# Optimization experiments

Hardware: AMD Instinct MI355X
Metric: run time of the kernel (lower is better)

The kernel has to match this reference:

```python
import jax, jax.numpy as jnp
import numpy as np

WIN = 7
K1, K2 = 0.01, 0.03


def _box_filter(x, w):
    """Valid-padding uniform box filter. x: (B, D, H, W); w: (1, 1, k, k)."""
    B, D, H, Wd = x.shape
    k = w.shape[-1]
    y = jax.lax.conv_general_dilated(
        x.reshape(B * D, 1, H, Wd), w, window_strides=(1, 1), padding='VALID',
        dimension_numbers=('NCHW', 'OIHW', 'NCHW'))
    return y.reshape(B, D, H - k + 1, Wd - k + 1)


def setup_inputs() -> dict:
    key = jax.random.key(0)
    kx, ky = jax.random.split(key)
    X = jax.random.uniform(kx, (4, 64, 256, 256), dtype=jnp.float32)
    Y = jax.random.uniform(ky, (4, 64, 256, 256), dtype=jnp.float32)
    w = jnp.ones((1, 1, WIN, WIN), dtype=jnp.float32) / (WIN * WIN)  # buffer self.w
    return {"X": X, "Y": Y, "w": w}


def reference(X, Y, w):
    data_range = 1.0
    C1 = (K1 * data_range) ** 2
    C2 = (K2 * data_range) ** 2
    NP = WIN * WIN
    cov_norm = NP / (NP - 1)

    ux = _box_filter(X, w)
    uy = _box_filter(Y, w)
    uxx = _box_filter(X * X, w)
    uyy = _box_filter(Y * Y, w)
    uxy = _box_filter(X * Y, w)

    vx = cov_norm * (uxx - ux * ux)
    vy = cov_norm * (uyy - uy * uy)
    vxy = cov_norm * (uxy - ux * uy)

    A1 = 2.0 * ux * uy + C1
    A2 = 2.0 * vxy + C2
    B1 = ux * ux + uy * uy + C1
    B2 = vx + vy + C2
    S = (A1 * A2) / (B1 * B2)  # (B, D, H', W')

    # Faithful to torch: ssim_per_slice[:, i] = S_i.mean() (mean over batch AND spatial),
    # then 1 - mean over depth, returned per batch element.
    slice_means = S.mean(axis=(0, 2, 3))  # (D,)
    loss = 1.0 - slice_means.mean()
    return jnp.full((X.shape[0],), loss, dtype=X.dtype)
```

## Files before the change

kernel.cpp:

```cpp
#include <hip/hip_runtime.h>

#define H 256
#define W 256
#define W4 (W / 4)
#define OWID 250
#define NIMG 256
#define BAND 10
#define NBANDS 25
#define NBLK (NBANDS * NIMG)
#define WPB 4

#define HWIN_ISSUE(S, P, B3, BW, CX, CY)      \
    P  = (S.x + S.y) + S.z;                   \
    B3 = __shfl_down(P, 1);                   \
    BW = __shfl_down(S.w, 1);                 \
    CX = __shfl_down(S.x, 2);                 \
    CY = __shfl_down(S.y, 2);

#define HWIN_FIN(S, P, B3, BW, CX, CY, WA)    \
    WA[0] = (P + S.w) + B3;                   \
    WA[1] = WA[0] - S.x + BW;                 \
    WA[2] = WA[1] - S.y + CX;                 \
    WA[3] = WA[2] - S.z + CY;

__global__ __launch_bounds__(256) void ssim_band_kernel(
    const float* __restrict__ X, const float* __restrict__ Y,
    float* __restrict__ partial)
{
    const int lane = threadIdx.x & 63;
    const int wave = threadIdx.x >> 6;
    const int band = blockIdx.x;
    const int img  = blockIdx.y * WPB + wave;
    const int r0 = band * BAND;

    const float4* Xp = (const float4*)X + ((size_t)img * H + r0) * W4 + lane;
    const float4* Yp = (const float4*)Y + ((size_t)img * H + r0) * W4 + lane;

    float4 sx, sy, sxx, syy, sxy;

    {
        float4 xv = Xp[0], yv = Yp[0];
        sx = xv; sy = yv;
        sxx = make_float4(xv.x * xv.x, xv.y * xv.y, xv.z * xv.z, xv.w * xv.w);
        syy = make_float4(yv.x * yv.x, yv.y * yv.y, yv.z * yv.z, yv.w * yv.w);
        sxy = make_float4(xv.x * yv.x, xv.y * yv.y, xv.z * yv.z, xv.w * yv.w);
        #pragma unroll
        for (int i = 1; i < 6; ++i) {
            float4 a = Xp[i * W4], b = Yp[i * W4];
            sx.x += a.x; sx.y += a.y; sx.z += a.z; sx.w += a.w;
            sy.x += b.x; sy.y += b.y; sy.z += b.z; sy.w += b.w;
            sxx.x = fmaf(a.x, a.x, sxx.x); sxx.y = fmaf(a.y, a.y, sxx.y);
            sxx.z = fmaf(a.z, a.z, sxx.z); sxx.w = fmaf(a.w, a.w, sxx.w);
            syy.x = fmaf(b.x, b.x, syy.x); syy.y = fmaf(b.y, b.y, syy.y);
            syy.z = fmaf(b.z, b.z, syy.z); syy.w = fmaf(b.w, b.w, syy.w);
            sxy.x = fmaf(a.x, b.x, sxy.x); sxy.y = fmaf(a.y, b.y, sxy.y);
            sxy.z = fmaf(a.z, b.z, sxy.z); sxy.w = fmaf(a.w, b.w, sxy.w);
        }
    }

    const float C1N  = 0.2401f;
    const float C2N  = 2.1609f;
    const float COV  = 49.0f / 48.0f;
    const float COV2 = 2.0f * COV;
    float lsum = 0.0f;

    #define SSIM_ROW(wx, wy, wxx, wyy, wxy)                                   \
    {                                                                         \
        _Pragma("unroll")                                                     \
        for (int s = 0; s < 4; ++s) {                                         \
            const float SX = wx[s], SY = wy[s];                               \
            const float t1 = SX * SY;                                         \
            const float t2 = SX * SX;                                         \
            const float t3 = SY * SY;                                         \
            const float A1 = 2.0f * t1 + C1N;                                 \
            const float B1 = (t2 + t3) + C1N;                                 \
            const float A2 = COV2 * (49.0f * wxy[s] - t1) + C2N;              \
            const float B2 = COV * (49.0f * (wxx[s] + wyy[s]) - (t2 + t3)) + C2N; \
            const float S = (A1 * A2) * __builtin_amdgcn_rcpf(B1 * B2);       \
            if (4 * lane + s < OWID) lsum += S;                               \
        }                                                                     \
    }

    #define HWIN_SSIM()                                                       \
    {                                                                         \
        float p0, b30, bw0, cx0, cy0;                                         \
        float p1, b31, bw1, cx1, cy1;                                         \
        float p2, b32, bw2, cx2, cy2;                                         \
        float p3, b33, bw3, cx3, cy3;                                         \
        float p4, b34, bw4, cx4, cy4;                                         \
        HWIN_ISSUE(sx,  p0, b30, bw0, cx0, cy0)                               \
        HWIN_ISSUE(sy,  p1, b31, bw1, cx1, cy1)                               \
        HWIN_ISSUE(sxx, p2, b32, bw2, cx2, cy2)                               \
        HWIN_ISSUE(syy, p3, b33, bw3, cx3, cy3)                               \
        HWIN_ISSUE(sxy, p4, b34, bw4, cx4, cy4)                               \
        float wx[4], wy[4], wxx[4], wyy[4], wxy[4];                           \
        HWIN_FIN(sx,  p0, b30, bw0, cx0, cy0, wx)                             \
        HWIN_FIN(sy,  p1, b31, bw1, cx1, cy1, wy)                             \
        HWIN_FIN(sxx, p2, b32, bw2, cx2, cy2, wxx)                            \
        HWIN_FIN(syy, p3, b33, bw3, cx3, cy3, wyy)                            \
        HWIN_FIN(sxy, p4, b34, bw4, cx4, cy4, wxy)                            \
        SSIM_ROW(wx, wy, wxx, wyy, wxy)                                       \
    }

    float4 xn = Xp[6 * W4], yn = Yp[6 * W4];
    float4 xnp = Xp[7 * W4], ynp = Yp[7 * W4];
    float4 xop = Xp[0],      yop = Yp[0];
    {
        sx.x += xn.x; sx.y += xn.y; sx.z += xn.z; sx.w += xn.w;
        sy.x += yn.x; sy.y += yn.y; sy.z += yn.z; sy.w += yn.w;
        sxx.x = fmaf(xn.x, xn.x, sxx.x); sxx.y = fmaf(xn.y, xn.y, sxx.y);
        sxx.z = fmaf(xn.z, xn.z, sxx.z); sxx.w = fmaf(xn.w, xn.w, sxx.w);
        syy.x = fmaf(yn.x, yn.x, syy.x); syy.y = fmaf(yn.y, yn.y, syy.y);
        syy.z = fmaf(yn.z, yn.z, syy.z); syy.w = fmaf(yn.w, yn.w, syy.w);
        sxy.x = fmaf(xn.x, yn.x, sxy.x); sxy.y = fmaf(xn.y, yn.y, sxy.y);
        sxy.z = fmaf(xn.z, yn.z, sxy.z); sxy.w = fmaf(xn.w, yn.w, sxy.w);
        HWIN_SSIM()
    }

    #pragma unroll 3
    for (int j = 1; j < BAND; ++j) {
        const float4 cxn = xnp, cyn = ynp, cxo = xop, cyo = yop;
        if (j + 1 < BAND) {
            xnp = Xp[(j + 7) * W4]; ynp = Yp[(j + 7) * W4];
            xop = Xp[j * W4];       yop = Yp[j * W4];
        }
        sx.x += cxn.x - cxo.x; sx.y += cxn.y - cxo.y;
        sx.z += cxn.z - cxo.z; sx.w += cxn.w - cxo.w;
        sy.x += cyn.x - cyo.x; sy.y += cyn.y - cyo.y;
        sy.z += cyn.z - cyo.z; sy.w += cyn.w - cyo.w;
        sxx.x += cxn.x * cxn.x - cxo.x * cxo.x;
        sxx.y += cxn.y * cxn.y - cxo.y * cxo.y;
        sxx.z += cxn.z * cxn.z - cxo.z * cxo.z;
        sxx.w += cxn.w * cxn.w - cxo.w * cxo.w;
        syy.x += cyn.x * cyn.x - cyo.x * cyo.x;
        syy.y += cyn.y * cyn.y - cyo.y * cyo.y;
        syy.z += cyn.z * cyn.z - cyo.z * cyo.z;
        syy.w += cyn.w * cyn.w - cyo.w * cyo.w;
        sxy.x += cxn.x * cyn.x - cxo.x * cyo.x;
        sxy.y += cxn.y * cyn.y - cxo.y * cyo.y;
        sxy.z += cxn.z * cyn.z - cxo.z * cyo.z;
        sxy.w += cxn.w * cyn.w - cxo.w * cyo.w;
        HWIN_SSIM()
    }

    #pragma unroll
    for (int off = 32; off > 0; off >>= 1)
        lsum += __shfl_down(lsum, off, 64);
    if (lane == 0) partial[img * NBANDS + band] = lsum;
}

__global__ __launch_bounds__(1024) void ssim_reduce_kernel(
    const float* __restrict__ partial, float* __restrict__ out)
{
    const int tid = threadIdx.x;
    double acc = 0.0;
    for (int i = tid; i < NBLK; i += 1024)
        acc += (double)partial[i];
    #pragma unroll
    for (int off = 32; off > 0; off >>= 1)
        acc += __shfl_down(acc, off, 64);
    __shared__ double wsumd[16];
    if ((tid & 63) == 0) wsumd[tid >> 6] = acc;
    __syncthreads();
    if (tid == 0) {
        double total = 0.0;
        #pragma unroll
        for (int i = 0; i < 16; ++i) total += wsumd[i];
        float loss = (float)(1.0 - total / 16000000.0);
        out[0] = loss; out[1] = loss; out[2] = loss; out[3] = loss;
    }
}

extern "C" void kernel_launch(void* const* d_in, const int* in_sizes, int n_in,
                              void* d_out, int out_size, void* d_ws, size_t ws_size,
                              hipStream_t stream) {
    const float* X = (const float*)d_in[0];
    const float* Y = (const float*)d_in[1];
    float* out = (float*)d_out;
    float* partial = (float*)d_ws;

    hipLaunchKernelGGL(ssim_band_kernel, dim3(NBANDS, NIMG / WPB), dim3(256), 0,
                       stream, X, Y, partial);
    hipLaunchKernelGGL(ssim_reduce_kernel, dim3(1), dim3(1024), 0, stream,
                       partial, out);
}
```

Measured before the change: 163.0 us.

## Replace cross-lane shuffles with redundant overlapping loads for horizontal window sums

Each lane now loads 10 contiguous columns (two float4s and a float2) per row and keeps 10-wide vertical running sums for all five statistics. The 7-wide horizontal window is then computed in registers instead of with wave shuffles. This removes the shuffle traffic and its latency, but each row is loaded 2.5x (redundantly, mostly from cache), the register footprint rises to about 50 accumulators, and the explicit software prefetch of the next and outgoing rows is dropped in favour of direct loads each iteration.

Result: slower. 178.6 us (+9.6%).

```diff
diff --git a/kernel.cpp b/kernel.cpp
--- a/kernel.cpp
+++ b/kernel.cpp
@@ -2,7 +2,6 @@
 
 #define H 256
 #define W 256
-#define W4 (W / 4)
 #define OWID 250
 #define NIMG 256
 #define BAND 10
@@ -10,18 +9,22 @@
 #define NBLK (NBANDS * NIMG)
 #define WPB 4
 
-#define HWIN_ISSUE(S, P, B3, BW, CX, CY)      \
-    P  = (S.x + S.y) + S.z;                   \
-    B3 = __shfl_down(P, 1);                   \
-    BW = __shfl_down(S.w, 1);                 \
-    CX = __shfl_down(S.x, 2);                 \
-    CY = __shfl_down(S.y, 2);
 
-#define HWIN_FIN(S, P, B3, BW, CX, CY, WA)    \
-    WA[0] = (P + S.w) + B3;                   \
-    WA[1] = WA[0] - S.x + BW;                 \
-    WA[2] = WA[1] - S.y + CX;                 \
-    WA[3] = WA[2] - S.z + CY;
+__device__ __forceinline__ void load10(const float* __restrict__ row,
+                                       int c0, int c1, int c2, float v[10]) {
+    float4 a = *(const float4*)(row + c0);
+    float4 b = *(const float4*)(row + c1);
+    float2 c = *(const float2*)(row + c2);
+    v[0] = a.x; v[1] = a.y; v[2] = a.z; v[3] = a.w;
+    v[4] = b.x; v[5] = b.y; v[6] = b.z; v[7] = b.w;
+    v[8] = c.x; v[9] = c.y;
+}
+
+#define HSUM(S, WA)                                                \
+    WA[0] = (((S[0] + S[1]) + (S[2] + S[3])) + ((S[4] + S[5]) + S[6])); \
+    WA[1] = WA[0] - S[0] + S[7];                                   \
+    WA[2] = WA[1] - S[1] + S[8];                                   \
+    WA[3] = WA[2] - S[2] + S[9];
 
 __global__ __launch_bounds__(256) void ssim_band_kernel(
     const float* __restrict__ X, const float* __restrict__ Y,
@@ -33,28 +36,38 @@
     const int img  = blockIdx.y * WPB + wave;
     const int r0 = band * BAND;
 
-    const float4* Xp = (const float4*)X + ((size_t)img * H + r0) * W4 + lane;
-    const float4* Yp = (const float4*)Y + ((size_t)img * H + r0) * W4 + lane;
+    const float* Xb = X + ((size_t)img * H + r0) * W;
+    const float* Yb = Y + ((size_t)img * H + r0) * W;
 
-    float4 sx, sy, sxx, syy, sxy;
+    const int c0 = 4 * lane;
+    const int c1 = (c0 + 4 < 252) ? c0 + 4 : 252;
+    const int c2 = (c0 + 8 < 254) ? c0 + 8 : 254;
+
+    float sx[10], sy[10], sxx[10], syy[10], sxy[10];
 
     {
-        float4 xv = Xp[0], yv = Yp[0];
-        sx = xv; sy = yv;
-        sxx = make_float4(xv.x * xv.x, xv.y * xv.y, xv.z * xv.z, xv.w * xv.w);
-        syy = make_float4(yv.x * yv.x, yv.y * yv.y, yv.z * yv.z, yv.w * yv.w);
-        sxy = make_float4(xv.x * yv.x, xv.y * yv.y, xv.z * yv.z, xv.w * yv.w);
+        float xv[10], yv[10];
+        load10(Xb, c0, c1, c2, xv);
+        load10(Yb, c0, c1, c2, yv);
         #pragma unroll
+        for (int k = 0; k < 10; ++k) {
+            sx[k] = xv[k]; sy[k] = yv[k];
+            sxx[k] = xv[k] * xv[k];
+            syy[k] = yv[k] * yv[k];
+            sxy[k] = xv[k] * yv[k];
+        }
+        #pragma unroll 2
         for (int i = 1; i < 6; ++i) {
-            float4 a = Xp[i * W4], b = Yp[i * W4];
-            sx.x += a.x; sx.y += a.y; sx.z += a.z; sx.w += a.w;
-            sy.x += b.x; sy.y += b.y; sy.z += b.z; sy.w += b.w;
-            sxx.x = fmaf(a.x, a.x, sxx.x); sxx.y = fmaf(a.y, a.y, sxx.y);
-            sxx.z = fmaf(a.z, a.z, sxx.z); sxx.w = fmaf(a.w, a.w, sxx.w);
-            syy.x = fmaf(b.x, b.x, syy.x); syy.y = fmaf(b.y, b.y, syy.y);
-            syy.z = fmaf(b.z, b.z, syy.z); syy.w = fmaf(b.w, b.w, syy.w);
-            sxy.x = fmaf(a.x, b.x, sxy.x); sxy.y = fmaf(a.y, b.y, sxy.y);
-            sxy.z = fmaf(a.z, b.z, sxy.z); sxy.w = fmaf(a.w, b.w, sxy.w);
+            load10(Xb + i * W, c0, c1, c2, xv);
+            load10(Yb + i * W, c0, c1, c2, yv);
+            #pragma unroll
+            for (int k = 0; k < 10; ++k) {
+                sx[k] += xv[k];
+                sy[k] += yv[k];
+                sxx[k] = fmaf(xv[k], xv[k], sxx[k]);
+                syy[k] = fmaf(yv[k], yv[k], syy[k]);
+                sxy[k] = fmaf(xv[k], yv[k], sxy[k]);
+            }
         }
     }
 
@@ -64,8 +77,14 @@
     const float COV2 = 2.0f * COV;
     float lsum = 0.0f;
 
-    #define SSIM_ROW(wx, wy, wxx, wyy, wxy)                                   \
+    #define HWIN_SSIM()                                                       \
     {                                                                         \
+        float wx[4], wy[4], wxx[4], wyy[4], wxy[4];                           \
+        HSUM(sx,  wx)                                                         \
+        HSUM(sy,  wy)                                                         \
+        HSUM(sxx, wxx)                                                        \
+        HSUM(syy, wyy)                                                        \
+        HSUM(sxy, wxy)                                                        \
         _Pragma("unroll")                                                     \
         for (int s = 0; s < 4; ++s) {                                         \
             const float SX = wx[s], SY = wy[s];                               \
@@ -77,69 +96,40 @@
             const float A2 = COV2 * (49.0f * wxy[s] - t1) + C2N;              \
             const float B2 = COV * (49.0f * (wxx[s] + wyy[s]) - (t2 + t3)) + C2N; \
             const float S = (A1 * A2) * __builtin_amdgcn_rcpf(B1 * B2);       \
-            if (4 * lane + s < OWID) lsum += S;                               \
+            if (c0 + s < OWID) lsum += S;                                     \
         }                                                                     \
     }
 
-    #define HWIN_SSIM()                                                       \
-    {                                                                         \
-        float p0, b30, bw0, cx0, cy0;                                         \
-        float p1, b31, bw1, cx1, cy1;                                         \
-        float p2, b32, bw2, cx2, cy2;                                         \
-        float p3, b33, bw3, cx3, cy3;                                         \
-        float p4, b34, bw4, cx4, cy4;                                         \
-        HWIN_ISSUE(sx,  p0, b30, bw0, cx0, cy0)                               \
-        HWIN_ISSUE(sy,  p1, b31, bw1, cx1, cy1)                               \
-        HWIN_ISSUE(sxx, p2, b32, bw2, cx2, cy2)                               \
-        HWIN_ISSUE(syy, p3, b33, bw3, cx3, cy3)                               \
-        HWIN_ISSUE(sxy, p4, b34, bw4, cx4, cy4)                               \
-        float wx[4], wy[4], wxx[4], wyy[4], wxy[4];                           \
-        HWIN_FIN(sx,  p0, b30, bw0, cx0, cy0, wx)                             \
-        HWIN_FIN(sy,  p1, b31, bw1, cx1, cy1, wy)                             \
-        HWIN_FIN(sxx, p2, b32, bw2, cx2, cy2, wxx)                            \
-        HWIN_FIN(syy, p3, b33, bw3, cx3, cy3, wyy)                            \
-        HWIN_FIN(sxy, p4, b34, bw4, cx4, cy4, wxy)                            \
-        SSIM_ROW(wx, wy, wxx, wyy, wxy)                                       \
-    }
-
-    float4 xn = Xp[6 * W4], yn = Yp[6 * W4];
-    float4 xnp = Xp[7 * W4], ynp = Yp[7 * W4];
-    float4 xop = Xp[0],      yop = Yp[0];
     {
-        sx.x += xn.x; sx.y += xn.y; sx.z += xn.z; sx.w += xn.w;
-        sy.x += yn.x; sy.y += yn.y; sy.z += yn.z; sy.w += yn.w;
-        sxx.x = fmaf(xn.x, xn.x, sxx.x); sxx.y = fmaf(xn.y, xn.y, sxx.y);
-        sxx.z = fmaf(xn.z, xn.z, sxx.z); sxx.w = fmaf(xn.w, xn.w, sxx.w);
-        syy.x = fmaf(yn.x, yn.x, syy.x); syy.y = fmaf(yn.y, yn.y, syy.y);
-        syy.z = fmaf(yn.z, yn.z, syy.z); syy.w = fmaf(yn.w, yn.w, syy.w);
-        sxy.x = fmaf(xn.x, yn.x, sxy.x); sxy.y = fmaf(xn.y, yn.y, sxy.y);
-        sxy.z = fmaf(xn.z, yn.z, sxy.z); sxy.w = fmaf(xn.w, yn.w, sxy.w);
+        float xn[10], yn[10];
+        load10(Xb + 6 * W, c0, c1, c2, xn);
+        load10(Yb + 6 * W, c0, c1, c2, yn);
+        #pragma unroll
+        for (int k = 0; k < 10; ++k) {
+            sx[k] += xn[k];
+            sy[k] += yn[k];
+            sxx[k] = fmaf(xn[k], xn[k], sxx[k]);
+            syy[k] = fmaf(yn[k], yn[k], syy[k]);
+            sxy[k] = fmaf(xn[k], yn[k], sxy[k]);
+        }
         HWIN_SSIM()
     }
 
     #pragma unroll 3
     for (int j = 1; j < BAND; ++j) {
-        const float4 cxn = xnp, cyn = ynp, cxo = xop, cyo = yop;
-        if (j + 1 < BAND) {
-            xnp = Xp[(j + 7) * W4]; ynp = Yp[(j + 7) * W4];
-            xop = Xp[j * W4];       yop = Yp[j * W4];
+        float xn[10], yn[10], xo[10], yo[10];
+        load10(Xb + (j + 6) * W, c0, c1, c2, xn);
+        load10(Yb + (j + 6) * W, c0, c1, c2, yn);
+        load10(Xb + (j - 1) * W, c0, c1, c2, xo);
+        load10(Yb + (j - 1) * W, c0, c1, c2, yo);
+        #pragma unroll
+        for (int k = 0; k < 10; ++k) {
+            sx[k] += xn[k] - xo[k];
+            sy[k] += yn[k] - yo[k];
+            sxx[k] += xn[k] * xn[k] - xo[k] * xo[k];
+            syy[k] += yn[k] * yn[k] - yo[k] * yo[k];
+            sxy[k] += xn[k] * yn[k] - xo[k] * yo[k];
         }
-        sx.x += cxn.x - cxo.x; sx.y += cxn.y - cxo.y;
-        sx.z += cxn.z - cxo.z; sx.w += cxn.w - cxo.w;
-        sy.x += cyn.x - cyo.x; sy.y += cyn.y - cyo.y;
-        sy.z += cyn.z - cyo.z; sy.w += cyn.w - cyo.w;
-        sxx.x += cxn.x * cxn.x - cxo.x * cxo.x;
-        sxx.y += cxn.y * cxn.y - cxo.y * cxo.y;
-        sxx.z += cxn.z * cxn.z - cxo.z * cxo.z;
-        sxx.w += cxn.w * cxn.w - cxo.w * cxo.w;
-        syy.x += cyn.x * cyn.x - cyo.x * cyo.x;
-        syy.y += cyn.y * cyn.y - cyo.y * cyo.y;
-        syy.z += cyn.z * cyn.z - cyo.z * cyo.z;
-        syy.w += cyn.w * cyn.w - cyo.w * cyo.w;
-        sxy.x += cxn.x * cyn.x - cxo.x * cyo.x;
-        sxy.y += cxn.y * cyn.y - cxo.y * cyo.y;
-        sxy.z += cxn.z * cyn.z - cxo.z * cyo.z;
-        sxy.w += cxn.w * cyn.w - cxo.w * cyo.w;
         HWIN_SSIM()
     }
 
```
